# Optimization experiments

Measured on AMD Instinct MI355X. Metric: run time of the kernel, lower is better.

Reference implementation:

```python
import jax, jax.numpy as jnp
import numpy as np

D_MODEL = 2048
NHEADS = 16
HEAD_DIM = D_MODEL // NHEADS


def setup_inputs() -> dict:
    key = jax.random.key(0)
    kx, kq, kk, kv, ko = jax.random.split(key, 5)
    B, S = 2, 2048
    scale = 1.0 / np.sqrt(D_MODEL)
    return {
        "x": jax.random.normal(kx, (B, S, D_MODEL), dtype=jnp.float32),
        "Wq": jax.random.normal(kq, (D_MODEL, D_MODEL), dtype=jnp.float32) * scale,
        "Wk": jax.random.normal(kk, (D_MODEL, D_MODEL), dtype=jnp.float32) * scale,
        "Wv": jax.random.normal(kv, (D_MODEL, D_MODEL), dtype=jnp.float32) * scale,
        "Wo": jax.random.normal(ko, (D_MODEL, D_MODEL), dtype=jnp.float32) * scale,
    }


def reference(x, Wq, Wk, Wv, Wo):
    B, S, _ = x.shape
    # nn.Linear(bias=False): y = x @ W.T
    q = (x @ Wq.T).reshape(B, S, NHEADS, HEAD_DIM)
    k = (x @ Wk.T).reshape(B, S, NHEADS, HEAD_DIM)
    v = (x @ Wv.T).reshape(B, S, NHEADS, HEAD_DIM)
    sm_scale = 1.0 / np.sqrt(HEAD_DIM)
    # scores: [B, H, S, S]
    scores = jnp.einsum("bqhd,bkhd->bhqk", q, k) * sm_scale
    causal_mask = jnp.tril(jnp.ones((S, S), dtype=bool))  # [S, S]
    scores = jnp.where(causal_mask, scores, jnp.finfo(scores.dtype).min)
    probs = jax.nn.softmax(scores, axis=-1)
    attn = jnp.einsum("bhqk,bkhd->bqhd", probs, v)  # [B, S, H, D]
    out = attn.reshape(B, S, D_MODEL) @ Wo.T
    return out
```

## Files before the change

### kernel.cpp

```cpp
#include <hip/hip_runtime.h>
#include <hip/hip_bf16.h>
#include <type_traits>

#define DEV __device__ __forceinline__

typedef __bf16 bf16x8 __attribute__((ext_vector_type(8)));
typedef float f32x4 __attribute__((ext_vector_type(4)));
typedef float f32x16 __attribute__((ext_vector_type(16)));
typedef unsigned short u16;
typedef unsigned int u32;

DEV u16 f32_to_bf16(float f) {
  union { float f; u32 u; } x; x.f = f;
  u32 r = (x.u + 0x7FFFu + ((x.u >> 16) & 1u)) >> 16;
  return (u16)r;
}

DEV u32 pack_bf16(float a, float b) {
  return (u32)f32_to_bf16(a) | ((u32)f32_to_bf16(b) << 16);
}

DEV void ld_lds16(const void* g, void* l) {
  __builtin_amdgcn_global_load_lds(
      (const __attribute__((address_space(1))) u32*)g,
      (__attribute__((address_space(3))) u32*)l, 16, 0, 0);
}

#define MFMA16(a, b, c) __builtin_amdgcn_mfma_f32_16x16x32_bf16(a, b, c, 0, 0, 0)
#define MFMA32(a, b, c) __builtin_amdgcn_mfma_f32_32x32x16_bf16(a, b, c, 0, 0, 0)

__global__ __launch_bounds__(256) void cast_kernel(const float* __restrict__ in,
                                                   u16* __restrict__ out, int n) {
  int i = (blockIdx.x * 256 + threadIdx.x) * 4;
  if (i >= n) return;
  float4 v = *reinterpret_cast<const float4*>(in + i);
  ushort4 o;
  o.x = f32_to_bf16(v.x); o.y = f32_to_bf16(v.y);
  o.z = f32_to_bf16(v.z); o.w = f32_to_bf16(v.w);
  *reinterpret_cast<ushort4*>(out + i) = o;
}

template <typename OutT>
__global__ __launch_bounds__(256) void gemm_nt(const u16* __restrict__ A,
                                               const u16* __restrict__ B,
                                               OutT* __restrict__ C,
                                               int M, int N, int K) {
  __shared__ __align__(16) u16 sA[128 * 64];
  __shared__ __align__(16) u16 sB[128 * 64];
  const int tid = threadIdx.x;
  const int lane = tid & 63, wid = tid >> 6;
  const int lo = lane & 15, hi = lane >> 4;
  const int wm = wid >> 1, wn = wid & 1;
  const int m0 = blockIdx.y * 128, n0 = blockIdx.x * 128;

  f32x4 acc[4][4] = {};

  for (int k0 = 0; k0 < K; k0 += 64) {
    __syncthreads();
#pragma unroll
    for (int i = 0; i < 4; ++i) {
      int e16 = i * 256 + tid;
      int r = e16 >> 3;
      int bcol = ((e16 & 7) * 16) ^ ((r & 7) << 4);
      int col = bcol >> 1;
      ld_lds16(A + (size_t)(m0 + r) * K + k0 + col, sA + e16 * 8);
      ld_lds16(B + (size_t)(n0 + r) * K + k0 + col, sB + e16 * 8);
    }
    __syncthreads();
#pragma unroll
    for (int kc = 0; kc < 2; ++kc) {
      bf16x8 a[4], b[4];
#pragma unroll
      for (int i = 0; i < 4; ++i) {
        int row = wm * 64 + i * 16 + lo;
        int boff = ((kc * 32 + hi * 8) * 2) ^ ((row & 7) << 4);
        a[i] = *(const bf16x8*)((const char*)sA + row * 128 + boff);
      }
#pragma unroll
      for (int i = 0; i < 4; ++i) {
        int row = wn * 64 + i * 16 + lo;
        int boff = ((kc * 32 + hi * 8) * 2) ^ ((row & 7) << 4);
        b[i] = *(const bf16x8*)((const char*)sB + row * 128 + boff);
      }
#pragma unroll
      for (int mi = 0; mi < 4; ++mi)
#pragma unroll
        for (int ni = 0; ni < 4; ++ni)
          acc[mi][ni] = MFMA16(a[mi], b[ni], acc[mi][ni]);
    }
  }
#pragma unroll
  for (int mi = 0; mi < 4; ++mi)
#pragma unroll
    for (int r = 0; r < 4; ++r) {
      size_t row = m0 + wm * 64 + mi * 16 + hi * 4 + r;
#pragma unroll
      for (int ni = 0; ni < 4; ++ni) {
        int col = n0 + wn * 64 + ni * 16 + lo;
        float v = acc[mi][ni][r];
        if constexpr (std::is_same<OutT, float>::value)
          C[row * N + col] = v;
        else
          C[row * N + col] = f32_to_bf16(v);
      }
    }
}

constexpr float SM_SCALE = 0.08838834764831845f;
constexpr float RTHR = 8.0f / SM_SCALE;

__global__ __launch_bounds__(256, 2) void attn_fwd(const u16* __restrict__ Q,
                                                   const u16* __restrict__ K,
                                                   const u16* __restrict__ VT,
                                                   u16* __restrict__ O) {
  __shared__ __align__(16) u16 sK[2][64 * 128];
  __shared__ __align__(16) u16 sV[2][128 * 64];

  const int x = blockIdx.x, h = blockIdx.y, b = blockIdx.z;
  const int qt = b ? x : (15 - x);
  const int tid = threadIdx.x;
  const int lane = tid & 63, wid = tid >> 6;
  const int l31 = lane & 31, hi5 = lane >> 5;

  const size_t baseQK = ((size_t)b * 2048) * 2048 + (size_t)h * 128;
  const size_t baseV  = ((size_t)h * 128) * 4096 + (size_t)b * 2048;
  const int q0 = qt * 128;
  const int qw = q0 + wid * 32;
  const int qg = qw + l31;
  const int nt = 2 * qt + 2;

  bf16x8 qf[8];
#pragma unroll
  for (int kc = 0; kc < 8; ++kc)
    qf[kc] = *(const bf16x8*)(Q + baseQK + (size_t)qg * 2048 + kc * 16 + hi5 * 8);

  f32x16 o[4] = {};
  float m = -INFINITY, ls = 0.f;

  auto stage = [&](int buf, int t) {
    const int kv = t * 64;
#pragma unroll
    for (int i = 0; i < 4; ++i) {
      int e = i * 256 + tid;
      int r = e >> 4;
      int bc = ((e & 15) * 16) ^ ((r & 7) << 4);
      ld_lds16(K + baseQK + (size_t)(kv + r) * 2048 + (bc >> 1), &sK[buf][e * 8]);
    }
#pragma unroll
    for (int i = 0; i < 4; ++i) {
      int e = i * 256 + tid;
      int r = e >> 3;
      int bc = ((e & 7) * 16) ^ ((r & 7) << 4);
      ld_lds16(VT + baseV + (size_t)r * 4096 + kv + (bc >> 1), &sV[buf][e * 8]);
    }
  };

  stage(0, 0);

  for (int t = 0; t < nt; ++t) {
    __syncthreads();
    if (t + 1 < nt) stage((t + 1) & 1, t + 1);
    const int kv0 = t * 64;
    if (kv0 > qw + 31) continue;
    const u16* bK = sK[t & 1];
    const u16* bV = sV[t & 1];

    f32x16 s[2] = {};
#pragma unroll
    for (int kb = 0; kb < 2; ++kb) {
      int row = kb * 32 + l31;
      int rsw = (row & 7) << 4;
#pragma unroll
      for (int kc = 0; kc < 8; ++kc) {
        int bo = (kc * 32 + hi5 * 16) ^ rsw;
        bf16x8 kf = *(const bf16x8*)((const char*)bK + row * 256 + bo);
        s[kb] = MFMA32(kf, qf[kc], s[kb]);
      }
    }

    if (kv0 + 63 > qw) {
#pragma unroll
      for (int kb = 0; kb < 2; ++kb)
#pragma unroll
        for (int j = 0; j < 16; ++j) {
          int keyg = kv0 + kb * 32 + (j & 3) + 8 * (j >> 2) + 4 * hi5;
          s[kb][j] = (keyg > qg) ? -3e38f : s[kb][j];
        }
    }

    float pmax = -3e38f;
#pragma unroll
    for (int kb = 0; kb < 2; ++kb)
#pragma unroll
      for (int j = 0; j < 16; ++j) pmax = fmaxf(pmax, s[kb][j]);
    pmax = fmaxf(pmax, __shfl_xor(pmax, 32));

    if (!__all(pmax - m <= RTHR)) {
      float mn = fmaxf(m, pmax);
      float fr = __expf((m - mn) * SM_SCALE);
      ls *= fr;
#pragma unroll
      for (int d = 0; d < 4; ++d) o[d] *= fr;
      m = mn;
    }

    float rs = 0.f;
#pragma unroll
    for (int kb = 0; kb < 2; ++kb)
#pragma unroll
      for (int j = 0; j < 16; ++j) {
        float p = __expf((s[kb][j] - m) * SM_SCALE);
        s[kb][j] = p;
        rs += p;
      }
    rs += __shfl_xor(rs, 32);
    ls += rs;

    union PF { u32 w[4]; bf16x8 v; };
    PF pf[4];
#pragma unroll
    for (int kb = 0; kb < 2; ++kb)
#pragma unroll
      for (int gp = 0; gp < 2; ++gp) {
        u32 keep[2], send[2];
#pragma unroll
        for (int w = 0; w < 2; ++w) {
          int ja = 8 * gp + 2 * w;
          int jb = 8 * gp + 4 + 2 * w;
          u32 aa = pack_bf16(s[kb][ja], s[kb][ja + 1]);
          u32 bb = pack_bf16(s[kb][jb], s[kb][jb + 1]);
          keep[w] = hi5 ? bb : aa;
          send[w] = hi5 ? aa : bb;
        }
        u32 recv0 = (u32)__shfl_xor((int)send[0], 32);
        u32 recv1 = (u32)__shfl_xor((int)send[1], 32);
        PF& f = pf[2 * kb + gp];
        f.w[0] = hi5 ? recv0 : keep[0];
        f.w[1] = hi5 ? recv1 : keep[1];
        f.w[2] = hi5 ? keep[0] : recv0;
        f.w[3] = hi5 ? keep[1] : recv1;
      }

#pragma unroll
    for (int d = 0; d < 4; ++d) {
      int row = d * 32 + l31;
      int rsw = (row & 7) << 4;
#pragma unroll
      for (int ks = 0; ks < 4; ++ks) {
        int bo = (ks * 32 + hi5 * 16) ^ rsw;
        bf16x8 vf = *(const bf16x8*)((const char*)bV + row * 128 + bo);
        o[d] = MFMA32(vf, pf[ks].v, o[d]);
      }
    }
  }

  float inv = 1.f / ls;
  size_t orow = (size_t)b * 2048 + qg;
#pragma unroll
  for (int d = 0; d < 4; ++d)
#pragma unroll
    for (int G = 0; G < 4; ++G) {
      ushort4 st;
      st.x = f32_to_bf16(o[d][4 * G + 0] * inv);
      st.y = f32_to_bf16(o[d][4 * G + 1] * inv);
      st.z = f32_to_bf16(o[d][4 * G + 2] * inv);
      st.w = f32_to_bf16(o[d][4 * G + 3] * inv);
      int col = h * 128 + d * 32 + 8 * G + 4 * hi5;
      *(ushort4*)(O + orow * 2048 + col) = st;
    }
}

extern "C" void kernel_launch(void* const* d_in, const int* in_sizes, int n_in,
                              void* d_out, int out_size, void* d_ws, size_t ws_size,
                              hipStream_t stream) {
  const float* x  = (const float*)d_in[0];
  const float* Wq = (const float*)d_in[1];
  const float* Wk = (const float*)d_in[2];
  const float* Wv = (const float*)d_in[3];
  const float* Wo = (const float*)d_in[4];
  float* out = (float*)d_out;

  constexpr int B = 2, S = 2048, D = 2048;
  constexpr int M = B * S;

  char* ws = (char*)d_ws;
  u16* xb  = (u16*)ws; ws += (size_t)M * D * 2;
  u16* wqb = (u16*)ws; ws += (size_t)D * D * 2;
  u16* wkb = (u16*)ws; ws += (size_t)D * D * 2;
  u16* wvb = (u16*)ws; ws += (size_t)D * D * 2;
  u16* wob = (u16*)ws; ws += (size_t)D * D * 2;
  u16* q   = (u16*)ws; ws += (size_t)M * D * 2;
  u16* k   = (u16*)ws; ws += (size_t)M * D * 2;
  u16* vT  = (u16*)ws; ws += (size_t)M * D * 2;
  u16* att = (u16*)ws; ws += (size_t)M * D * 2;

  cast_kernel<<<M * D / 1024, 256, 0, stream>>>(x, xb, M * D);
  cast_kernel<<<D * D / 1024, 256, 0, stream>>>(Wq, wqb, D * D);
  cast_kernel<<<D * D / 1024, 256, 0, stream>>>(Wk, wkb, D * D);
  cast_kernel<<<D * D / 1024, 256, 0, stream>>>(Wv, wvb, D * D);
  cast_kernel<<<D * D / 1024, 256, 0, stream>>>(Wo, wob, D * D);

  dim3 gg(D / 128, M / 128);
  gemm_nt<u16><<<gg, 256, 0, stream>>>(xb, wqb, q, M, D, D);
  gemm_nt<u16><<<gg, 256, 0, stream>>>(xb, wkb, k, M, D, D);
  gemm_nt<u16><<<dim3(M / 128, D / 128), 256, 0, stream>>>(wvb, xb, vT, D, M, D);

  attn_fwd<<<dim3(16, 16, B), 256, 0, stream>>>(q, k, vT, att);

  gemm_nt<float><<<gg, 256, 0, stream>>>(att, wob, out, M, D, D);
}
```

Before: 278.3 us.

## Pair causal q-tiles per 512-thread block, fold softmax scale into Q, use exp2

The attention grid drops to 8 blocks of 512 threads. Each block pairs a short and a long causal q-tile that share the same K/V staging, which balances work across blocks and halves redundant K/V loads. The softmax scale times log2(e) is folded into the Q projection epilogue, so the kernel can use exp2 without per-element scale multiplies. bf16 packing now uses the native float2-to-bf16x2 conversion, and s_setprio is raised around the MFMA sections. In exchange, Q is rounded to bf16 after scaling, and the 512-thread blocks with 2 blocks per CU put more pressure on registers.

```diff
diff --git a/kernel.cpp b/kernel.cpp
--- a/kernel.cpp
+++ b/kernel.cpp
@@ -16,8 +16,10 @@
   return (u16)r;
 }
 
-DEV u32 pack_bf16(float a, float b) {
-  return (u32)f32_to_bf16(a) | ((u32)f32_to_bf16(b) << 16);
+DEV u32 pack2(float a, float b) {
+  union { __hip_bfloat162 h; u32 u; } c;
+  c.h = __float22bfloat162_rn(float2{a, b});
+  return c.u;
 }
 
 DEV void ld_lds16(const void* g, void* l) {
@@ -44,7 +46,7 @@
 __global__ __launch_bounds__(256) void gemm_nt(const u16* __restrict__ A,
                                                const u16* __restrict__ B,
                                                OutT* __restrict__ C,
-                                               int M, int N, int K) {
+                                               int M, int N, int K, float osc) {
   __shared__ __align__(16) u16 sA[128 * 64];
   __shared__ __align__(16) u16 sB[128 * 64];
   const int tid = threadIdx.x;
@@ -97,7 +99,7 @@
 #pragma unroll
       for (int ni = 0; ni < 4; ++ni) {
         int col = n0 + wn * 64 + ni * 16 + lo;
-        float v = acc[mi][ni][r];
+        float v = acc[mi][ni][r] * osc;
         if constexpr (std::is_same<OutT, float>::value)
           C[row * N + col] = v;
         else
@@ -106,28 +108,27 @@
     }
 }
 
-constexpr float SM_SCALE = 0.08838834764831845f;
-constexpr float RTHR = 8.0f / SM_SCALE;
-
-__global__ __launch_bounds__(256, 2) void attn_fwd(const u16* __restrict__ Q,
+constexpr float RTHR2 = 11.5416f;
+
+__global__ __launch_bounds__(512, 2) void attn_fwd(const u16* __restrict__ Q,
                                                    const u16* __restrict__ K,
                                                    const u16* __restrict__ VT,
                                                    u16* __restrict__ O) {
   __shared__ __align__(16) u16 sK[2][64 * 128];
   __shared__ __align__(16) u16 sV[2][128 * 64];
 
-  const int x = blockIdx.x, h = blockIdx.y, b = blockIdx.z;
-  const int qt = b ? x : (15 - x);
+  const int p = blockIdx.x, h = blockIdx.y, b = blockIdx.z;
   const int tid = threadIdx.x;
   const int lane = tid & 63, wid = tid >> 6;
   const int l31 = lane & 31, hi5 = lane >> 5;
+  const int g = wid >> 2;
+  const int qt = g ? p : (15 - p);
+  const int qw = qt * 128 + (wid & 3) * 32;
+  const int qg = qw + l31;
+  const int nt = 2 * (15 - p) + 2;
 
   const size_t baseQK = ((size_t)b * 2048) * 2048 + (size_t)h * 128;
   const size_t baseV  = ((size_t)h * 128) * 4096 + (size_t)b * 2048;
-  const int q0 = qt * 128;
-  const int qw = q0 + wid * 32;
-  const int qg = qw + l31;
-  const int nt = 2 * qt + 2;
 
   bf16x8 qf[8];
 #pragma unroll
@@ -140,15 +141,15 @@
   auto stage = [&](int buf, int t) {
     const int kv = t * 64;
 #pragma unroll
-    for (int i = 0; i < 4; ++i) {
-      int e = i * 256 + tid;
+    for (int i = 0; i < 2; ++i) {
+      int e = i * 512 + tid;
       int r = e >> 4;
       int bc = ((e & 15) * 16) ^ ((r & 7) << 4);
       ld_lds16(K + baseQK + (size_t)(kv + r) * 2048 + (bc >> 1), &sK[buf][e * 8]);
     }
 #pragma unroll
-    for (int i = 0; i < 4; ++i) {
-      int e = i * 256 + tid;
+    for (int i = 0; i < 2; ++i) {
+      int e = i * 512 + tid;
       int r = e >> 3;
       int bc = ((e & 7) * 16) ^ ((r & 7) << 4);
       ld_lds16(VT + baseV + (size_t)r * 4096 + kv + (bc >> 1), &sV[buf][e * 8]);
@@ -166,6 +167,7 @@
     const u16* bV = sV[t & 1];
 
     f32x16 s[2] = {};
+    __builtin_amdgcn_s_setprio(1);
 #pragma unroll
     for (int kb = 0; kb < 2; ++kb) {
       int row = kb * 32 + l31;
@@ -177,6 +179,7 @@
         s[kb] = MFMA32(kf, qf[kc], s[kb]);
       }
     }
+    __builtin_amdgcn_s_setprio(0);
 
     if (kv0 + 63 > qw) {
 #pragma unroll
@@ -195,9 +198,9 @@
       for (int j = 0; j < 16; ++j) pmax = fmaxf(pmax, s[kb][j]);
     pmax = fmaxf(pmax, __shfl_xor(pmax, 32));
 
-    if (!__all(pmax - m <= RTHR)) {
+    if (!__all(pmax - m <= RTHR2)) {
       float mn = fmaxf(m, pmax);
-      float fr = __expf((m - mn) * SM_SCALE);
+      float fr = exp2f(m - mn);
       ls *= fr;
 #pragma unroll
       for (int d = 0; d < 4; ++d) o[d] *= fr;
@@ -209,9 +212,9 @@
     for (int kb = 0; kb < 2; ++kb)
 #pragma unroll
       for (int j = 0; j < 16; ++j) {
-        float p = __expf((s[kb][j] - m) * SM_SCALE);
-        s[kb][j] = p;
-        rs += p;
+        float pv = exp2f(s[kb][j] - m);
+        s[kb][j] = pv;
+        rs += pv;
       }
     rs += __shfl_xor(rs, 32);
     ls += rs;
@@ -227,8 +230,8 @@
         for (int w = 0; w < 2; ++w) {
           int ja = 8 * gp + 2 * w;
           int jb = 8 * gp + 4 + 2 * w;
-          u32 aa = pack_bf16(s[kb][ja], s[kb][ja + 1]);
-          u32 bb = pack_bf16(s[kb][jb], s[kb][jb + 1]);
+          u32 aa = pack2(s[kb][ja], s[kb][ja + 1]);
+          u32 bb = pack2(s[kb][jb], s[kb][jb + 1]);
           keep[w] = hi5 ? bb : aa;
           send[w] = hi5 ? aa : bb;
         }
@@ -241,6 +244,7 @@
         f.w[3] = hi5 ? keep[1] : recv1;
       }
 
+    __builtin_amdgcn_s_setprio(1);
 #pragma unroll
     for (int d = 0; d < 4; ++d) {
       int row = d * 32 + l31;
@@ -252,6 +256,7 @@
         o[d] = MFMA32(vf, pf[ks].v, o[d]);
       }
     }
+    __builtin_amdgcn_s_setprio(0);
   }
 
   float inv = 1.f / ls;
@@ -260,13 +265,11 @@
   for (int d = 0; d < 4; ++d)
 #pragma unroll
     for (int G = 0; G < 4; ++G) {
-      ushort4 st;
-      st.x = f32_to_bf16(o[d][4 * G + 0] * inv);
-      st.y = f32_to_bf16(o[d][4 * G + 1] * inv);
-      st.z = f32_to_bf16(o[d][4 * G + 2] * inv);
-      st.w = f32_to_bf16(o[d][4 * G + 3] * inv);
+      union { u32 u[2]; ushort4 s4; } st;
+      st.u[0] = pack2(o[d][4 * G + 0] * inv, o[d][4 * G + 1] * inv);
+      st.u[1] = pack2(o[d][4 * G + 2] * inv, o[d][4 * G + 3] * inv);
       int col = h * 128 + d * 32 + 8 * G + 4 * hi5;
-      *(ushort4*)(O + orow * 2048 + col) = st;
+      *(ushort4*)(O + orow * 2048 + col) = st.s4;
     }
 }
 
@@ -282,6 +285,7 @@
 
   constexpr int B = 2, S = 2048, D = 2048;
   constexpr int M = B * S;
+  constexpr float QSC = 0.12751742f;
 
   char* ws = (char*)d_ws;
   u16* xb  = (u16*)ws; ws += (size_t)M * D * 2;
@@ -301,11 +305,11 @@
   cast_kernel<<<D * D / 1024, 256, 0, stream>>>(Wo, wob, D * D);
 
   dim3 gg(D / 128, M / 128);
-  gemm_nt<u16><<<gg, 256, 0, stream>>>(xb, wqb, q, M, D, D);
-  gemm_nt<u16><<<gg, 256, 0, stream>>>(xb, wkb, k, M, D, D);
-  gemm_nt<u16><<<dim3(M / 128, D / 128), 256, 0, stream>>>(wvb, xb, vT, D, M, D);
-
-  attn_fwd<<<dim3(16, 16, B), 256, 0, stream>>>(q, k, vT, att);
-
-  gemm_nt<float><<<gg, 256, 0, stream>>>(att, wob, out, M, D, D);
-}
+  gemm_nt<u16><<<gg, 256, 0, stream>>>(xb, wqb, q, M, D, D, QSC);
+  gemm_nt<u16><<<gg, 256, 0, stream>>>(xb, wkb, k, M, D, D, 1.0f);
+  gemm_nt<u16><<<dim3(M / 128, D / 128), 256, 0, stream>>>(wvb, xb, vT, D, M, D, 1.0f);
+
+  attn_fwd<<<dim3(8, 16, B), 512, 0, stream>>>(q, k, vT, att);
+
+  gemm_nt<float><<<gg, 256, 0, stream>>>(att, wob, out, M, D, D, 1.0f);
+}
```

New measurement: 286.8 us. 1.03x slower.
